# Optimization experiments

Measured on AMD Instinct MI355X. Metric: run time of the kernel, lower is better.

The kernel has to match this reference:

```python
import jax, jax.numpy as jnp
import numpy as np

D_MODEL = 1024
D_FF = 4096          # shared expert hidden
NUM_M = 2
E_ROUTER = 8 * NUM_M - 1   # 15 router experts
D_FF_R = D_FF // NUM_M     # 2048 router expert hidden
TOP_K = NUM_M * 2 - 1      # 3
B, T = 2, 2048


def setup_inputs() -> dict:
    key = jax.random.key(0)
    ks = jax.random.split(key, 12)
    s = lambda fan_in: 1.0 / np.sqrt(fan_in)
    x = jax.random.normal(ks[0], (B, T, D_MODEL), dtype=jnp.float32)
    # shared experts stacked [S=1, ...]
    sW1 = jax.random.uniform(ks[1], (1, D_MODEL, D_FF), jnp.float32, -s(D_MODEL), s(D_MODEL))
    sb1 = jax.random.uniform(ks[2], (1, D_FF), jnp.float32, -s(D_MODEL), s(D_MODEL))
    sW2 = jax.random.uniform(ks[3], (1, D_FF, D_MODEL), jnp.float32, -s(D_FF), s(D_FF))
    sb2 = jax.random.uniform(ks[4], (1, D_MODEL), jnp.float32, -s(D_FF), s(D_FF))
    # router experts stacked [E, ...]
    rW1 = jax.random.uniform(ks[5], (E_ROUTER, D_MODEL, D_FF_R), jnp.float32, -s(D_MODEL), s(D_MODEL))
    rb1 = jax.random.uniform(ks[6], (E_ROUTER, D_FF_R), jnp.float32, -s(D_MODEL), s(D_MODEL))
    rW2 = jax.random.uniform(ks[7], (E_ROUTER, D_FF_R, D_MODEL), jnp.float32, -s(D_FF_R), s(D_FF_R))
    rb2 = jax.random.uniform(ks[8], (E_ROUTER, D_MODEL), jnp.float32, -s(D_FF_R), s(D_FF_R))
    # gating linear d_model -> E
    gW = jax.random.uniform(ks[9], (D_MODEL, E_ROUTER), jnp.float32, -s(D_MODEL), s(D_MODEL))
    gb = jax.random.uniform(ks[10], (E_ROUTER,), jnp.float32, -s(D_MODEL), s(D_MODEL))
    return {"x": x, "sW1": sW1, "sb1": sb1, "sW2": sW2, "sb2": sb2,
            "rW1": rW1, "rb1": rb1, "rW2": rW2, "rb2": rb2, "gW": gW, "gb": gb}


def _expert_stack(x, W1, b1, W2, b2):
    # x: [b,t,d]; W1: [e,d,f] -> out [e,b,t,d]
    h = jax.nn.gelu(jnp.einsum('btd,edf->ebtf', x, W1) + b1[:, None, None, :],
                    approximate=False)
    return jnp.einsum('ebtf,efd->ebtd', h, W2) + b2[:, None, None, :]


def reference(x, sW1, sb1, sW2, sb2, rW1, rb1, rW2, rb2, gW, gb):
    # shared experts (sum over S)
    shared_enc = _expert_stack(x, sW1, sb1, sW2, sb2).sum(0)  # [b,t,d]
    # gating: softmax then keep top-k values (no renormalization)
    weights = jax.nn.softmax(x @ gW + gb, axis=-1)            # [b,t,E]
    topv, topi = jax.lax.top_k(weights, TOP_K)                # [b,t,K]
    gated = (jax.nn.one_hot(topi, E_ROUTER, dtype=weights.dtype)
             * topv[..., None]).sum(axis=-2)                  # [b,t,E]
    # dense per-expert compute masked by sparse gates (faithful to source)
    router_out = _expert_stack(x, rW1, rb1, rW2, rb2)         # [E,b,t,d]
    router_enc = jnp.einsum('ebtd,bte->btd', router_out, gated)
    return shared_enc + router_enc + x
```

## Files before the change

kernel.cpp:

```cpp
#include <hip/hip_runtime.h>
#include <hip/hip_bf16.h>
#include <cstdint>
#include <cstddef>

#define TOKENS 4096
#define DM     1024
#define DFF    4096
#define NE     15
#define DFR    2048
#define NEX    17
#define MAXT   104

typedef float f32x4 __attribute__((ext_vector_type(4)));
typedef int   i32x4 __attribute__((ext_vector_type(4)));

__device__ __forceinline__ void mfma_16x16x32_bf16(f32x4& d, i32x4 a, i32x4 b){
  asm("v_mfma_f32_16x16x32_bf16 %0, %1, %2, %0" : "+v"(d) : "v"(a), "v"(b));
}

__device__ __forceinline__ void gload16(const void* g, void* l){
  __builtin_amdgcn_global_load_lds(
      (const __attribute__((address_space(1))) uint32_t*)g,
      (__attribute__((address_space(3))) uint32_t*)l, 16, 0, 0);
}

__device__ __forceinline__ unsigned short f2bf(float f){
  unsigned u = __float_as_uint(f);
  u += 0x7FFFu + ((u >> 16) & 1u);
  return (unsigned short)(u >> 16);
}

__device__ __forceinline__ float gelu_exact(float v){
  return 0.5f * v * (1.0f + erff(v * 0.70710678118654752440f));
}


__global__ void cast_x_kernel(const float* __restrict__ x, ushort* __restrict__ xb, int n4){
  int i = blockIdx.x*256 + threadIdx.x;
  if (i >= n4) return;
  float4 v = reinterpret_cast<const float4*>(x)[i];
  ushort4 o; o.x=f2bf(v.x); o.y=f2bf(v.y); o.z=f2bf(v.z); o.w=f2bf(v.w);
  reinterpret_cast<ushort4*>(xb)[i] = o;
}

__global__ void tcast_kernel(const float* __restrict__ src, ushort* __restrict__ dst, int R, int C){
  __shared__ float tile[32][33];
  const size_t bo = (size_t)blockIdx.z * R * C;
  const int c0 = blockIdx.x*32, r0 = blockIdx.y*32;
  const int tx = threadIdx.x, ty = threadIdx.y;
  #pragma unroll
  for (int i=0;i<4;i++){
    int r = ty + i*8;
    tile[r][tx] = src[bo + (size_t)(r0+r)*C + c0 + tx];
  }
  __syncthreads();
  #pragma unroll
  for (int i=0;i<4;i++){
    int r = ty + i*8;
    dst[bo + (size_t)(c0+r)*R + r0 + tx] = f2bf(tile[tx][r]);
  }
}


__global__ void gate_kernel(const float* __restrict__ x, const float* __restrict__ gW,
                            const float* __restrict__ gb,
                            int* __restrict__ tokexp, float* __restrict__ tokp){
  const int wave = threadIdx.x >> 6, lane = threadIdx.x & 63;
  const int token = blockIdx.x*4 + wave;
  const float* xr = x + (size_t)token * DM;
  float a[NE];
  #pragma unroll
  for (int e=0;e<NE;e++) a[e] = 0.f;
  const int d0 = lane * 16;
  float xv[16];
  #pragma unroll
  for (int j=0;j<4;j++){
    float4 v = reinterpret_cast<const float4*>(xr + d0)[j];
    xv[j*4+0]=v.x; xv[j*4+1]=v.y; xv[j*4+2]=v.z; xv[j*4+3]=v.w;
  }
  for (int j=0;j<16;j++){
    const float* gr = gW + (size_t)(d0 + j) * NE;
    #pragma unroll
    for (int e=0;e<NE;e++) a[e] += xv[j]*gr[e];
  }
  #pragma unroll
  for (int e=0;e<NE;e++){
    for (int off=32; off; off>>=1) a[e] += __shfl_xor(a[e], off, 64);
  }
  if (lane == 0){
    float l[NE], p[NE];
    float m = -1e30f;
    for (int e=0;e<NE;e++){ l[e] = a[e] + gb[e]; m = fmaxf(m, l[e]); }
    float s = 0.f;
    for (int e=0;e<NE;e++){ p[e] = expf(l[e]-m); s += p[e]; }
    float inv = 1.f/s;
    unsigned used = 0;
    for (int k=0;k<3;k++){
      int best = -1; float bv = -1e30f;
      for (int e=0;e<NE;e++) if (!((used>>e)&1u) && l[e] > bv){ bv = l[e]; best = e; }
      used |= 1u<<best;
      tokexp[token*3 + k] = best;
      tokp[token*3 + k]   = p[best]*inv;
    }
  }
}


__global__ void assign_kernel(const int* __restrict__ tokexp, const float* __restrict__ tokp,
                              int* __restrict__ counts, int* __restrict__ bases,
                              int* __restrict__ tokidx, float* __restrict__ gatev,
                              int* __restrict__ tokslot,
                              int* __restrict__ tile_e, int* __restrict__ tile_by,
                              int* __restrict__ ntiles){
  __shared__ int lh[256][NE];
  const int tid = threadIdx.x;
  const int t0 = tid * 16;

  int le[48];
  #pragma unroll
  for (int e=0;e<NE;e++) lh[tid][e] = 0;
  #pragma unroll
  for (int j=0;j<48;j++){
    int e = tokexp[t0*3 + j];
    le[j] = e;
    lh[tid][e]++;
  }
  __syncthreads();
  if (tid < NE){
    int run = 0;
    for (int i=0;i<256;i++){
      int v = lh[i][tid];
      lh[i][tid] = run;
      run += v;
    }
    counts[tid] = run;
  }
  __syncthreads();
  if (tid == 0){
    int b = 0;
    int t = 0;
    for (int e=0;e<NE;e++){
      int c = counts[e];
      int prows = ((c+127)>>7)<<7;
      bases[e] = b; b += prows;
      int nb = (prows + 255) >> 8;
      for (int j=0;j<nb && t<MAXT;j++){ tile_e[t]=e; tile_by[t]=j; t++; }
    }
    bases[NE] = b; bases[NE+1] = b + TOKENS;
    for (int e=NE;e<NEX;e++){
      for (int j=0;j<16 && t<MAXT;j++){ tile_e[t]=e; tile_by[t]=j; t++; }
    }
    ntiles[0] = t;
  }
  __syncthreads();
  #pragma unroll
  for (int j=0;j<48;j++){
    const int t = t0 + (j/3), k = j - (j/3)*3;
    const int e = le[j];
    const int slot = lh[tid][e]++;
    const int idx = e*TOKENS + slot;
    tokidx[idx] = t;
    gatev[idx]  = tokp[t*3 + k];
    tokslot[t*3 + k] = idx;
  }
}


#define GEMM_COMPUTE(BASEB)                                                          \
  {                                                                                  \
    const char* gbase = (BASEB);                                                     \
    _Pragma("unroll")                                                                \
    for (int p=0; p<4; ++p){                                                         \
      const int qr = p>>1, qc = p&1;                                                 \
      i32x4 af[2][4], bf[2][2];                                                      \
      _Pragma("unroll")                                                              \
      for (int kk=0; kk<2; kk++){                                                    \
        const unsigned cb = (unsigned)((kk*64 + ((lane>>4)<<4)) ^ sw);               \
        _Pragma("unroll")                                                            \
        for (int m=0;m<4;m++){                                                       \
          const int row = wr*128 + qr*64 + m*16 + (lane&15);                         \
          af[kk][m] = *(const i32x4*)(gbase + row*128 + cb);                         \
        }                                                                            \
        _Pragma("unroll")                                                            \
        for (int n=0;n<2;n++){                                                       \
          const int row = wc*64 + qc*32 + n*16 + (lane&15);                          \
          bf[kk][n] = *(const i32x4*)(gbase + 32768 + row*128 + cb);                 \
        }                                                                            \
      }                                                                              \
      __builtin_amdgcn_s_setprio(1);                                                 \
      _Pragma("unroll")                                                              \
      for (int m=0;m<4;m++){                                                         \
        _Pragma("unroll")                                                            \
        for (int n=0;n<2;n++){                                                       \
          mfma_16x16x32_bf16(acc[qr*4+m][qc*2+n], af[0][m], bf[0][n]);               \
          mfma_16x16x32_bf16(acc[qr*4+m][qc*2+n], af[1][m], bf[1][n]);               \
        }                                                                            \
      }                                                                              \
      __builtin_amdgcn_s_setprio(0);                                                 \
    }                                                                                \
  }

#define GEMM_STAGE(BUF, T)                                                           \
  {                                                                                  \
    char* dA = smem + (size_t)(BUF)*65536;                                           \
    char* dB = dA + 32768;                                                           \
    _Pragma("unroll")                                                                \
    for (int i=0;i<4;i++){                                                           \
      gload16(aSrc[i] + (size_t)(T)*128, dA + i*8192 + tid*16);                      \
      gload16(bSrc[i] + (size_t)(T)*128, dB + i*8192 + tid*16);                      \
    }                                                                                \
  }


__global__ __launch_bounds__(512,2) void gemm1_kernel(
    const ushort* __restrict__ xb, const ushort* __restrict__ rW1T,
    const ushort* __restrict__ sW1T, const float* __restrict__ rb1,
    const float* __restrict__ sb1, const int* __restrict__ counts,
    const int* __restrict__ bases, const int* __restrict__ tokidx,
    const int* __restrict__ tile_e, const int* __restrict__ tile_by,
    const int* __restrict__ ntiles, ushort* __restrict__ h)
{
  const int ty = blockIdx.y;
  if (ty >= ntiles[0]) return;
  const int e = tile_e[ty], by = tile_by[ty], bx = blockIdx.x;
  const int cnt = (e < NE) ? counts[e] : TOKENS;
  const int prows = (e < NE) ? (((cnt+127)>>7)<<7) : TOKENS;

  __shared__ __align__(16) char smem[131072];

  const int tid = threadIdx.x;
  const int wave = tid >> 6, lane = tid & 63;
  const int wr = wave >> 2, wc = wave & 3;
  const unsigned sw = (unsigned)((lane & 7) << 4);

  const char* Bpb = (e < NE) ? (const char*)rW1T + ((size_t)e*DFR)*2048
                             : (const char*)sW1T + ((size_t)(e-NE)*DFR)*2048;

  const unsigned scol = (unsigned)(((tid & 7) << 4) ^ (((tid >> 3) & 7) << 4));
  const char* aSrc[4];
  const char* bSrc[4];
  #pragma unroll
  for (int i=0;i<4;i++){
    const int rl = i*64 + (tid >> 3);
    const int gr = by*256 + rl;
    int tok;
    if (e < NE){ const int cr = gr < cnt ? gr : cnt-1; tok = tokidx[e*TOKENS + cr]; }
    else       { tok = gr < TOKENS ? gr : TOKENS-1; }
    aSrc[i] = (const char*)xb + (size_t)tok*2048 + scol;
    bSrc[i] = Bpb + (size_t)(bx*256 + rl)*2048 + scol;
  }

  f32x4 acc[8][4];
  #pragma unroll
  for (int m=0;m<8;m++){
    #pragma unroll
    for (int n=0;n<4;n++){ acc[m][n] = (f32x4){0.f,0.f,0.f,0.f}; }
  }

  const int NK = DM/64;
  GEMM_STAGE(0, 0);
  asm volatile("s_waitcnt vmcnt(0)" ::: "memory");
  __builtin_amdgcn_s_barrier();
  #pragma unroll 2
  for (int t=0; t<NK-1; ++t){
    GEMM_STAGE((t+1)&1, t+1);
    asm volatile("s_waitcnt vmcnt(8)" ::: "memory");
    __builtin_amdgcn_s_barrier();
    GEMM_COMPUTE(smem + (size_t)(t&1)*65536);
    __builtin_amdgcn_s_barrier();
  }
  asm volatile("s_waitcnt vmcnt(0)" ::: "memory");
  __builtin_amdgcn_s_barrier();
  GEMM_COMPUTE(smem + (size_t)((NK-1)&1)*65536);

  const int hb = bases[e];
  const float* b1p = (e < NE) ? (rb1 + e*DFR + bx*256) : (sb1 + (e-NE)*DFR + bx*256);
  #pragma unroll
  for (int m=0;m<8;m++){
    const int rt = wr*128 + m*16 + (lane>>4)*4;
    #pragma unroll
    for (int i=0;i<4;i++){
      const int gr = by*256 + rt + i;
      if (gr < prows){
        #pragma unroll
        for (int n=0;n<4;n++){
          const int c = wc*64 + n*16 + (lane & 15);
          float v = acc[m][n][i] + b1p[c];
          h[(size_t)(hb + gr)*DFR + (size_t)bx*256 + c] = f2bf(gelu_exact(v));
        }
      }
    }
  }
}


__global__ __launch_bounds__(512,2) void gemm2_kernel(
    const ushort* __restrict__ hbuf, const ushort* __restrict__ rW2T,
    const ushort* __restrict__ sW2T, const float* __restrict__ rb2,
    const float* __restrict__ sb2, const int* __restrict__ counts,
    const int* __restrict__ bases,
    const int* __restrict__ tile_e, const int* __restrict__ tile_by,
    const int* __restrict__ ntiles, ushort* __restrict__ rout)
{
  const int ty = blockIdx.y;
  if (ty >= ntiles[0]) return;
  const int e = tile_e[ty], by = tile_by[ty], bx = blockIdx.x;
  const int cnt = (e < NE) ? counts[e] : TOKENS;
  const int prows = (e < NE) ? (((cnt+127)>>7)<<7) : TOKENS;
  const int hb = bases[e];

  __shared__ __align__(16) char smem[131072];

  const int tid = threadIdx.x;
  const int wave = tid >> 6, lane = tid & 63;
  const int wr = wave >> 2, wc = wave & 3;
  const unsigned sw = (unsigned)((lane & 7) << 4);

  const unsigned scol = (unsigned)(((tid & 7) << 4) ^ (((tid >> 3) & 7) << 4));
  const char* aSrc[4];
  const char* bSrc[4];
  #pragma unroll
  for (int i=0;i<4;i++){
    const int rl = i*64 + (tid >> 3);
    int ar = by*256 + rl; if (ar >= prows) ar = prows-1;
    aSrc[i] = (const char*)hbuf + (size_t)(hb + ar)*4096 + scol;
    if (e < NE){
      bSrc[i] = (const char*)rW2T + ((size_t)e*DM + bx*256 + rl)*4096 + scol;
    } else {
      bSrc[i] = (const char*)sW2T + (size_t)(bx*256 + rl)*8192 + (size_t)(e-NE)*4096 + scol;
    }
  }

  f32x4 acc[8][4];
  #pragma unroll
  for (int m=0;m<8;m++){
    #pragma unroll
    for (int n=0;n<4;n++){ acc[m][n] = (f32x4){0.f,0.f,0.f,0.f}; }
  }

  const int NK = DFR/64;
  GEMM_STAGE(0, 0);
  asm volatile("s_waitcnt vmcnt(0)" ::: "memory");
  __builtin_amdgcn_s_barrier();
  #pragma unroll 2
  for (int t=0; t<NK-1; ++t){
    GEMM_STAGE((t+1)&1, t+1);
    asm volatile("s_waitcnt vmcnt(8)" ::: "memory");
    __builtin_amdgcn_s_barrier();
    GEMM_COMPUTE(smem + (size_t)(t&1)*65536);
    __builtin_amdgcn_s_barrier();
  }
  asm volatile("s_waitcnt vmcnt(0)" ::: "memory");
  __builtin_amdgcn_s_barrier();
  GEMM_COMPUTE(smem + (size_t)((NK-1)&1)*65536);

  #pragma unroll
  for (int m=0;m<8;m++){
    const int rt = wr*128 + m*16 + (lane>>4)*4;
    #pragma unroll
    for (int i=0;i<4;i++){
      const int gr = by*256 + rt + i;
      if (gr < prows){
        #pragma unroll
        for (int n=0;n<4;n++){
          const int c  = wc*64 + n*16 + (lane & 15);
          const int cg = bx*256 + c;
          const float bias = (e < NE) ? rb2[e*DM + cg] : ((e == NE) ? sb2[cg] : 0.f);
          rout[(size_t)(hb + gr)*DM + cg] = f2bf(acc[m][n][i] + bias);
        }
      }
    }
  }
}


__global__ void combine_kernel(const float* __restrict__ x, const ushort* __restrict__ rout,
                               const int* __restrict__ bases, const int* __restrict__ tokslot,
                               const float* __restrict__ gatev, float* __restrict__ out)
{
  const int wave = threadIdx.x >> 6, lane = threadIdx.x & 63;
  const int token = blockIdx.x*4 + wave;
  const int d0 = lane*16;

  float acc[16];
  #pragma unroll
  for (int j=0;j<4;j++){
    float4 v = reinterpret_cast<const float4*>(x + (size_t)token*DM + d0)[j];
    acc[j*4+0]=v.x; acc[j*4+1]=v.y; acc[j*4+2]=v.z; acc[j*4+3]=v.w;
  }

  int   rows[5];
  float gs[5];
  rows[0] = bases[NE]   + token; gs[0] = 1.f;
  rows[1] = bases[NE+1] + token; gs[1] = 1.f;
  #pragma unroll
  for (int k=0;k<3;k++){
    const int idx = tokslot[token*3 + k];
    const int e = idx >> 12, s = idx & (TOKENS-1);
    rows[2+k] = bases[e] + s;
    gs[2+k] = gatev[idx];
  }

  #pragma unroll
  for (int q=0;q<5;q++){
    const float g = gs[q];
    const ushort* rp = rout + (size_t)rows[q]*DM + d0;
    #pragma unroll
    for (int h=0;h<2;h++){
      i32x4 v = *reinterpret_cast<const i32x4*>(rp + h*8);
      #pragma unroll
      for (int j=0;j<4;j++){
        const unsigned u = (unsigned)v[j];
        acc[h*8 + j*2 + 0] += g * __uint_as_float(u << 16);
        acc[h*8 + j*2 + 1] += g * __uint_as_float(u & 0xFFFF0000u);
      }
    }
  }

  #pragma unroll
  for (int j=0;j<4;j++){
    float4 v; v.x=acc[j*4+0]; v.y=acc[j*4+1]; v.z=acc[j*4+2]; v.w=acc[j*4+3];
    reinterpret_cast<float4*>(out + (size_t)token*DM + d0)[j] = v;
  }
}


extern "C" void kernel_launch(void* const* d_in, const int* in_sizes, int n_in,
                              void* d_out, int out_size, void* d_ws, size_t ws_size,
                              hipStream_t stream)
{
  (void)in_sizes; (void)n_in; (void)out_size; (void)ws_size;
  const float* x   = (const float*)d_in[0];
  const float* sW1 = (const float*)d_in[1];
  const float* sb1 = (const float*)d_in[2];
  const float* sW2 = (const float*)d_in[3];
  const float* sb2 = (const float*)d_in[4];
  const float* rW1 = (const float*)d_in[5];
  const float* rb1 = (const float*)d_in[6];
  const float* rW2 = (const float*)d_in[7];
  const float* rb2 = (const float*)d_in[8];
  const float* gW  = (const float*)d_in[9];
  const float* gb  = (const float*)d_in[10];
  float* out = (float*)d_out;

  char* ws = (char*)d_ws;
  ushort* xb   = (ushort*)(ws + 0);
  ushort* sW1T = (ushort*)(ws + 8388608);
  ushort* sW2T = (ushort*)(ws + 16777216);
  ushort* rW1T = (ushort*)(ws + 25165824);
  ushort* rW2T = (ushort*)(ws + 88080384);
  ushort* hbuf = (ushort*)(ws + 150994944);
  ushort* rout = (ushort*)(ws + 25165824);
  int*   counts  = (int*)(ws + 243269632);
  int*   bases   = (int*)(ws + 243269760);
  int*   tokidx  = (int*)(ws + 243270144);
  float* gatev   = (float*)(ws + 243515904);
  int*   tokslot = (int*)(ws + 243761664);
  int*   tokexp  = (int*)(ws + 243810816);
  float* tokp    = (float*)(ws + 243859968);
  int*   tile_e  = (int*)(ws + 243909120);
  int*   tile_by = (int*)(ws + 243910144);
  int*   ntiles  = (int*)(ws + 243911168);

  cast_x_kernel<<<dim3(TOKENS*DM/4/256), dim3(256), 0, stream>>>(x, xb, TOKENS*DM/4);
  tcast_kernel<<<dim3(DFF/32, DM/32, 1),  dim3(32,8), 0, stream>>>(sW1, sW1T, DM, DFF);
  tcast_kernel<<<dim3(DM/32, DFF/32, 1),  dim3(32,8), 0, stream>>>(sW2, sW2T, DFF, DM);
  tcast_kernel<<<dim3(DFR/32, DM/32, NE), dim3(32,8), 0, stream>>>(rW1, rW1T, DM, DFR);
  tcast_kernel<<<dim3(DM/32, DFR/32, NE), dim3(32,8), 0, stream>>>(rW2, rW2T, DFR, DM);

  gate_kernel<<<dim3(TOKENS/4), dim3(256), 0, stream>>>(x, gW, gb, tokexp, tokp);
  assign_kernel<<<dim3(1), dim3(256), 0, stream>>>(tokexp, tokp, counts, bases,
                                                   tokidx, gatev, tokslot,
                                                   tile_e, tile_by, ntiles);

  gemm1_kernel<<<dim3(8,MAXT), dim3(512), 0, stream>>>(
      xb, rW1T, sW1T, rb1, sb1, counts, bases, tokidx, tile_e, tile_by, ntiles, hbuf);
  gemm2_kernel<<<dim3(4,MAXT), dim3(512), 0, stream>>>(
      hbuf, rW2T, sW2T, rb2, sb2, counts, bases, tile_e, tile_by, ntiles, rout);
  combine_kernel<<<dim3(TOKENS/4), dim3(256), 0, stream>>>(
      x, rout, bases, tokslot, gatev, out);
}
```

Measured before the change: 491.9 us.

## Triple-buffer GEMM K-loop with smaller K tiles and 128-row gemm2 tiles

Both grouped GEMMs now use a three-stage LDS ring with K-step 32 instead of a two-stage ring with K-step 64. This keeps two loads in flight and needs only one barrier per iteration. gemm2 switches to 128-row M tiles with a separate tile list and launch bounds of 4, aiming for more blocks and higher occupancy and less padding waste. In exchange, the smaller K step adds more barriers and less MFMA work per sync, and gemm2 loses reuse of the B tile.

After: 450.9 us. -8.4%, faster.

```diff
diff --git a/kernel.cpp b/kernel.cpp
--- a/kernel.cpp
+++ b/kernel.cpp
@@ -10,6 +10,7 @@
 #define DFR    2048
 #define NEX    17
 #define MAXT   104
+#define MAXT2  176
 
 typedef float f32x4 __attribute__((ext_vector_type(4)));
 typedef int   i32x4 __attribute__((ext_vector_type(4)));
@@ -111,6 +112,7 @@
                               int* __restrict__ tokidx, float* __restrict__ gatev,
                               int* __restrict__ tokslot,
                               int* __restrict__ tile_e, int* __restrict__ tile_by,
+                              int* __restrict__ tile2_e, int* __restrict__ tile2_by,
                               int* __restrict__ ntiles){
   __shared__ int lh[256][NE];
   const int tid = threadIdx.x;
@@ -137,20 +139,22 @@
   }
   __syncthreads();
   if (tid == 0){
-    int b = 0;
-    int t = 0;
+    int b = 0, t1 = 0, t2 = 0;
     for (int e=0;e<NE;e++){
       int c = counts[e];
       int prows = ((c+127)>>7)<<7;
       bases[e] = b; b += prows;
-      int nb = (prows + 255) >> 8;
-      for (int j=0;j<nb && t<MAXT;j++){ tile_e[t]=e; tile_by[t]=j; t++; }
+      int nb1 = (prows + 255) >> 8;
+      for (int j=0;j<nb1 && t1<MAXT;j++){ tile_e[t1]=e; tile_by[t1]=j; t1++; }
+      int nb2 = prows >> 7;
+      for (int j=0;j<nb2 && t2<MAXT2;j++){ tile2_e[t2]=e; tile2_by[t2]=j; t2++; }
     }
     bases[NE] = b; bases[NE+1] = b + TOKENS;
     for (int e=NE;e<NEX;e++){
-      for (int j=0;j<16 && t<MAXT;j++){ tile_e[t]=e; tile_by[t]=j; t++; }
-    }
-    ntiles[0] = t;
+      for (int j=0;j<16 && t1<MAXT;j++){ tile_e[t1]=e; tile_by[t1]=j; t1++; }
+      for (int j=0;j<32 && t2<MAXT2;j++){ tile2_e[t2]=e; tile2_by[t2]=j; t2++; }
+    }
+    ntiles[0] = t1; ntiles[1] = t2;
   }
   __syncthreads();
   #pragma unroll
@@ -164,52 +168,6 @@
     tokslot[t*3 + k] = idx;
   }
 }
-
-
-#define GEMM_COMPUTE(BASEB)                                                          \
-  {                                                                                  \
-    const char* gbase = (BASEB);                                                     \
-    _Pragma("unroll")                                                                \
-    for (int p=0; p<4; ++p){                                                         \
-      const int qr = p>>1, qc = p&1;                                                 \
-      i32x4 af[2][4], bf[2][2];                                                      \
-      _Pragma("unroll")                                                              \
-      for (int kk=0; kk<2; kk++){                                                    \
-        const unsigned cb = (unsigned)((kk*64 + ((lane>>4)<<4)) ^ sw);               \
-        _Pragma("unroll")                                                            \
-        for (int m=0;m<4;m++){                                                       \
-          const int row = wr*128 + qr*64 + m*16 + (lane&15);                         \
-          af[kk][m] = *(const i32x4*)(gbase + row*128 + cb);                         \
-        }                                                                            \
-        _Pragma("unroll")                                                            \
-        for (int n=0;n<2;n++){                                                       \
-          const int row = wc*64 + qc*32 + n*16 + (lane&15);                          \
-          bf[kk][n] = *(const i32x4*)(gbase + 32768 + row*128 + cb);                 \
-        }                                                                            \
-      }                                                                              \
-      __builtin_amdgcn_s_setprio(1);                                                 \
-      _Pragma("unroll")                                                              \
-      for (int m=0;m<4;m++){                                                         \
-        _Pragma("unroll")                                                            \
-        for (int n=0;n<2;n++){                                                       \
-          mfma_16x16x32_bf16(acc[qr*4+m][qc*2+n], af[0][m], bf[0][n]);               \
-          mfma_16x16x32_bf16(acc[qr*4+m][qc*2+n], af[1][m], bf[1][n]);               \
-        }                                                                            \
-      }                                                                              \
-      __builtin_amdgcn_s_setprio(0);                                                 \
-    }                                                                                \
-  }
-
-#define GEMM_STAGE(BUF, T)                                                           \
-  {                                                                                  \
-    char* dA = smem + (size_t)(BUF)*65536;                                           \
-    char* dB = dA + 32768;                                                           \
-    _Pragma("unroll")                                                                \
-    for (int i=0;i<4;i++){                                                           \
-      gload16(aSrc[i] + (size_t)(T)*128, dA + i*8192 + tid*16);                      \
-      gload16(bSrc[i] + (size_t)(T)*128, dB + i*8192 + tid*16);                      \
-    }                                                                                \
-  }
 
 
 __global__ __launch_bounds__(512,2) void gemm1_kernel(
@@ -226,28 +184,26 @@
   const int cnt = (e < NE) ? counts[e] : TOKENS;
   const int prows = (e < NE) ? (((cnt+127)>>7)<<7) : TOKENS;
 
-  __shared__ __align__(16) char smem[131072];
-
-  const int tid = threadIdx.x;
-  const int wave = tid >> 6, lane = tid & 63;
+  __shared__ __align__(16) char smem[98304];
+
+  const int tid = threadIdx.x, wave = tid >> 6, lane = tid & 63;
   const int wr = wave >> 2, wc = wave & 3;
-  const unsigned sw = (unsigned)((lane & 7) << 4);
-
-  const char* Bpb = (e < NE) ? (const char*)rW1T + ((size_t)e*DFR)*2048
-                             : (const char*)sW1T + ((size_t)(e-NE)*DFR)*2048;
-
-  const unsigned scol = (unsigned)(((tid & 7) << 4) ^ (((tid >> 3) & 7) << 4));
-  const char* aSrc[4];
-  const char* bSrc[4];
-  #pragma unroll
-  for (int i=0;i<4;i++){
-    const int rl = i*64 + (tid >> 3);
+  const unsigned sc = (unsigned)(((tid & 3) ^ ((tid >> 3) & 3)) << 4);
+
+  const char* Bpb = (e < NE) ? (const char*)rW1T + (size_t)e*DFR*2048
+                             : (const char*)sW1T + (size_t)(e-NE)*DFR*2048;
+
+  const char* aSrc[2];
+  const char* bSrc[2];
+  #pragma unroll
+  for (int i=0;i<2;i++){
+    const int rl = i*128 + (tid>>2);
     const int gr = by*256 + rl;
     int tok;
     if (e < NE){ const int cr = gr < cnt ? gr : cnt-1; tok = tokidx[e*TOKENS + cr]; }
     else       { tok = gr < TOKENS ? gr : TOKENS-1; }
-    aSrc[i] = (const char*)xb + (size_t)tok*2048 + scol;
-    bSrc[i] = Bpb + (size_t)(bx*256 + rl)*2048 + scol;
+    aSrc[i] = (const char*)xb + (size_t)tok*2048 + sc;
+    bSrc[i] = Bpb + (size_t)(bx*256 + rl)*2048 + sc;
   }
 
   f32x4 acc[8][4];
@@ -257,21 +213,59 @@
     for (int n=0;n<4;n++){ acc[m][n] = (f32x4){0.f,0.f,0.f,0.f}; }
   }
 
-  const int NK = DM/64;
-  GEMM_STAGE(0, 0);
-  asm volatile("s_waitcnt vmcnt(0)" ::: "memory");
+#define G1_STAGE(BUF, T)                                                   \
+  { char* bp = smem + (BUF)*32768;                                         \
+    gload16(aSrc[0] + (T)*64, bp + tid*16);                                \
+    gload16(aSrc[1] + (T)*64, bp + 8192 + tid*16);                         \
+    gload16(bSrc[0] + (T)*64, bp + 16384 + tid*16);                        \
+    gload16(bSrc[1] + (T)*64, bp + 24576 + tid*16); }
+
+#define G1_COMPUTE(BUF)                                                    \
+  { const char* bp = smem + (BUF)*32768;                                   \
+    i32x4 bf[4];                                                           \
+    _Pragma("unroll")                                                      \
+    for (int n=0;n<4;n++){                                                 \
+      const int row = wc*64 + n*16 + (lane&15);                            \
+      bf[n] = *(const i32x4*)(bp + 16384 + row*64                          \
+               + (((lane>>4) ^ ((row>>1)&3))<<4));                         \
+    }                                                                      \
+    _Pragma("unroll")                                                      \
+    for (int q=0;q<2;q++){                                                 \
+      i32x4 af[4];                                                         \
+      _Pragma("unroll")                                                    \
+      for (int m=0;m<4;m++){                                               \
+        const int row = wr*128 + q*64 + m*16 + (lane&15);                  \
+        af[m] = *(const i32x4*)(bp + row*64                                \
+                 + (((lane>>4) ^ ((row>>1)&3))<<4));                       \
+      }                                                                    \
+      __builtin_amdgcn_s_setprio(1);                                       \
+      _Pragma("unroll")                                                    \
+      for (int m=0;m<4;m++){                                               \
+        _Pragma("unroll")                                                  \
+        for (int n=0;n<4;n++){ mfma_16x16x32_bf16(acc[q*4+m][n], af[m], bf[n]); } \
+      }                                                                    \
+      __builtin_amdgcn_s_setprio(0);                                       \
+    } }
+
+  const int NK = DM/32;
+  G1_STAGE(0, 0);
+  G1_STAGE(1, 1);
+  asm volatile("s_waitcnt vmcnt(4)" ::: "memory");
   __builtin_amdgcn_s_barrier();
-  #pragma unroll 2
-  for (int t=0; t<NK-1; ++t){
-    GEMM_STAGE((t+1)&1, t+1);
-    asm volatile("s_waitcnt vmcnt(8)" ::: "memory");
-    __builtin_amdgcn_s_barrier();
-    GEMM_COMPUTE(smem + (size_t)(t&1)*65536);
-    __builtin_amdgcn_s_barrier();
-  }
-  asm volatile("s_waitcnt vmcnt(0)" ::: "memory");
-  __builtin_amdgcn_s_barrier();
-  GEMM_COMPUTE(smem + (size_t)((NK-1)&1)*65536);
+  int cb = 0;
+  for (int t=0; t<NK; ++t){
+    if (t+2 < NK){
+      const int pb = (cb >= 1) ? cb-1 : cb+2;
+      G1_STAGE(pb, t+2);
+    }
+    G1_COMPUTE(cb);
+    if (t < NK-1){
+      if (t+2 < NK) asm volatile("s_waitcnt vmcnt(4)" ::: "memory");
+      else          asm volatile("s_waitcnt vmcnt(0)" ::: "memory");
+      __builtin_amdgcn_s_barrier();
+    }
+    cb = (cb==2) ? 0 : cb+1;
+  }
 
   const int hb = bases[e];
   const float* b1p = (e < NE) ? (rb1 + e*DFR + bx*256) : (sb1 + (e-NE)*DFR + bx*256);
@@ -291,75 +285,108 @@
       }
     }
   }
-}
-
-
-__global__ __launch_bounds__(512,2) void gemm2_kernel(
+#undef G1_STAGE
+#undef G1_COMPUTE
+}
+
+
+__global__ __launch_bounds__(512,4) void gemm2_kernel(
     const ushort* __restrict__ hbuf, const ushort* __restrict__ rW2T,
     const ushort* __restrict__ sW2T, const float* __restrict__ rb2,
     const float* __restrict__ sb2, const int* __restrict__ counts,
     const int* __restrict__ bases,
-    const int* __restrict__ tile_e, const int* __restrict__ tile_by,
+    const int* __restrict__ tile2_e, const int* __restrict__ tile2_by,
     const int* __restrict__ ntiles, ushort* __restrict__ rout)
 {
   const int ty = blockIdx.y;
-  if (ty >= ntiles[0]) return;
-  const int e = tile_e[ty], by = tile_by[ty], bx = blockIdx.x;
+  if (ty >= ntiles[1]) return;
+  const int e = tile2_e[ty], by = tile2_by[ty], bx = blockIdx.x;
   const int cnt = (e < NE) ? counts[e] : TOKENS;
   const int prows = (e < NE) ? (((cnt+127)>>7)<<7) : TOKENS;
   const int hb = bases[e];
 
-  __shared__ __align__(16) char smem[131072];
-
-  const int tid = threadIdx.x;
-  const int wave = tid >> 6, lane = tid & 63;
+  __shared__ __align__(16) char smem[73728];
+
+  const int tid = threadIdx.x, wave = tid >> 6, lane = tid & 63;
   const int wr = wave >> 2, wc = wave & 3;
-  const unsigned sw = (unsigned)((lane & 7) << 4);
-
-  const unsigned scol = (unsigned)(((tid & 7) << 4) ^ (((tid >> 3) & 7) << 4));
-  const char* aSrc[4];
-  const char* bSrc[4];
-  #pragma unroll
-  for (int i=0;i<4;i++){
-    const int rl = i*64 + (tid >> 3);
-    int ar = by*256 + rl; if (ar >= prows) ar = prows-1;
-    aSrc[i] = (const char*)hbuf + (size_t)(hb + ar)*4096 + scol;
-    if (e < NE){
-      bSrc[i] = (const char*)rW2T + ((size_t)e*DM + bx*256 + rl)*4096 + scol;
-    } else {
-      bSrc[i] = (const char*)sW2T + (size_t)(bx*256 + rl)*8192 + (size_t)(e-NE)*4096 + scol;
-    }
-  }
-
-  f32x4 acc[8][4];
-  #pragma unroll
-  for (int m=0;m<8;m++){
+  const unsigned sc = (unsigned)(((tid & 3) ^ ((tid >> 3) & 3)) << 4);
+
+  const char* aSrc;
+  {
+    const int rl = tid>>2;
+    int ar = by*128 + rl; if (ar >= prows) ar = prows-1;
+    aSrc = (const char*)hbuf + (size_t)(hb + ar)*4096 + sc;
+  }
+  const char* bSrc[2];
+  #pragma unroll
+  for (int i=0;i<2;i++){
+    const int rl = i*128 + (tid>>2);
+    if (e < NE) bSrc[i] = (const char*)rW2T + ((size_t)e*DM + bx*256 + rl)*4096 + sc;
+    else        bSrc[i] = (const char*)sW2T + (size_t)(bx*256 + rl)*8192 + (size_t)(e-NE)*4096 + sc;
+  }
+
+  f32x4 acc[4][4];
+  #pragma unroll
+  for (int m=0;m<4;m++){
     #pragma unroll
     for (int n=0;n<4;n++){ acc[m][n] = (f32x4){0.f,0.f,0.f,0.f}; }
   }
 
-  const int NK = DFR/64;
-  GEMM_STAGE(0, 0);
-  asm volatile("s_waitcnt vmcnt(0)" ::: "memory");
+#define G2_STAGE(BUF, T)                                                   \
+  { char* bp = smem + (BUF)*24576;                                         \
+    gload16(aSrc + (T)*64, bp + tid*16);                                   \
+    gload16(bSrc[0] + (T)*64, bp + 8192 + tid*16);                         \
+    gload16(bSrc[1] + (T)*64, bp + 16384 + tid*16); }
+
+#define G2_COMPUTE(BUF)                                                    \
+  { const char* bp = smem + (BUF)*24576;                                   \
+    i32x4 bf[4], af[4];                                                    \
+    _Pragma("unroll")                                                      \
+    for (int n=0;n<4;n++){                                                 \
+      const int row = wc*64 + n*16 + (lane&15);                            \
+      bf[n] = *(const i32x4*)(bp + 8192 + row*64                           \
+               + (((lane>>4) ^ ((row>>1)&3))<<4));                         \
+    }                                                                      \
+    _Pragma("unroll")                                                      \
+    for (int m=0;m<4;m++){                                                 \
+      const int row = wr*64 + m*16 + (lane&15);                            \
+      af[m] = *(const i32x4*)(bp + row*64                                  \
+               + (((lane>>4) ^ ((row>>1)&3))<<4));                         \
+    }                                                                      \
+    __builtin_amdgcn_s_setprio(1);                                         \
+    _Pragma("unroll")                                                      \
+    for (int m=0;m<4;m++){                                                 \
+      _Pragma("unroll")                                                    \
+      for (int n=0;n<4;n++){ mfma_16x16x32_bf16(acc[m][n], af[m], bf[n]); }\
+    }                                                                      \
+    __builtin_amdgcn_s_setprio(0); }
+
+  const int NK = DFR/32;
+  G2_STAGE(0, 0);
+  G2_STAGE(1, 1);
+  asm volatile("s_waitcnt vmcnt(3)" ::: "memory");
   __builtin_amdgcn_s_barrier();
-  #pragma unroll 2
-  for (int t=0; t<NK-1; ++t){
-    GEMM_STAGE((t+1)&1, t+1);
-    asm volatile("s_waitcnt vmcnt(8)" ::: "memory");
-    __builtin_amdgcn_s_barrier();
-    GEMM_COMPUTE(smem + (size_t)(t&1)*65536);
-    __builtin_amdgcn_s_barrier();
-  }
-  asm volatile("s_waitcnt vmcnt(0)" ::: "memory");
-  __builtin_amdgcn_s_barrier();
-  GEMM_COMPUTE(smem + (size_t)((NK-1)&1)*65536);
-
-  #pragma unroll
-  for (int m=0;m<8;m++){
-    const int rt = wr*128 + m*16 + (lane>>4)*4;
+  int cb = 0;
+  for (int t=0; t<NK; ++t){
+    if (t+2 < NK){
+      const int pb = (cb >= 1) ? cb-1 : cb+2;
+      G2_STAGE(pb, t+2);
+    }
+    G2_COMPUTE(cb);
+    if (t < NK-1){
+      if (t+2 < NK) asm volatile("s_waitcnt vmcnt(3)" ::: "memory");
+      else          asm volatile("s_waitcnt vmcnt(0)" ::: "memory");
+      __builtin_amdgcn_s_barrier();
+    }
+    cb = (cb==2) ? 0 : cb+1;
+  }
+
+  #pragma unroll
+  for (int m=0;m<4;m++){
+    const int rt = wr*64 + m*16 + (lane>>4)*4;
     #pragma unroll
     for (int i=0;i<4;i++){
-      const int gr = by*256 + rt + i;
+      const int gr = by*128 + rt + i;
       if (gr < prows){
         #pragma unroll
         for (int n=0;n<4;n++){
@@ -371,6 +398,8 @@
       }
     }
   }
+#undef G2_STAGE
+#undef G2_COMPUTE
 }
 
 
@@ -406,13 +435,13 @@
     const float g = gs[q];
     const ushort* rp = rout + (size_t)rows[q]*DM + d0;
     #pragma unroll
-    for (int h=0;h<2;h++){
-      i32x4 v = *reinterpret_cast<const i32x4*>(rp + h*8);
+    for (int hh=0;hh<2;hh++){
+      i32x4 v = *reinterpret_cast<const i32x4*>(rp + hh*8);
       #pragma unroll
       for (int j=0;j<4;j++){
         const unsigned u = (unsigned)v[j];
-        acc[h*8 + j*2 + 0] += g * __uint_as_float(u << 16);
-        acc[h*8 + j*2 + 1] += g * __uint_as_float(u & 0xFFFF0000u);
+        acc[hh*8 + j*2 + 0] += g * __uint_as_float(u << 16);
+        acc[hh*8 + j*2 + 1] += g * __uint_as_float(u & 0xFFFF0000u);
       }
     }
   }
@@ -461,6 +490,8 @@
   int*   tile_e  = (int*)(ws + 243909120);
   int*   tile_by = (int*)(ws + 243910144);
   int*   ntiles  = (int*)(ws + 243911168);
+  int*   tile2_e = (int*)(ws + 243912192);
+  int*   tile2_by= (int*)(ws + 243913216);
 
   cast_x_kernel<<<dim3(TOKENS*DM/4/256), dim3(256), 0, stream>>>(x, xb, TOKENS*DM/4);
   tcast_kernel<<<dim3(DFF/32, DM/32, 1),  dim3(32,8), 0, stream>>>(sW1, sW1T, DM, DFF);
@@ -471,12 +502,12 @@
   gate_kernel<<<dim3(TOKENS/4), dim3(256), 0, stream>>>(x, gW, gb, tokexp, tokp);
   assign_kernel<<<dim3(1), dim3(256), 0, stream>>>(tokexp, tokp, counts, bases,
                                                    tokidx, gatev, tokslot,
-                                                   tile_e, tile_by, ntiles);
+                                                   tile_e, tile_by, tile2_e, tile2_by, ntiles);
 
   gemm1_kernel<<<dim3(8,MAXT), dim3(512), 0, stream>>>(
       xb, rW1T, sW1T, rb1, sb1, counts, bases, tokidx, tile_e, tile_by, ntiles, hbuf);
-  gemm2_kernel<<<dim3(4,MAXT), dim3(512), 0, stream>>>(
-      hbuf, rW2T, sW2T, rb2, sb2, counts, bases, tile_e, tile_by, ntiles, rout);
+  gemm2_kernel<<<dim3(4,MAXT2), dim3(512), 0, stream>>>(
+      hbuf, rW2T, sW2T, rb2, sb2, counts, bases, tile2_e, tile2_by, ntiles, rout);
   combine_kernel<<<dim3(TOKENS/4), dim3(256), 0, stream>>>(
       x, rout, bases, tokslot, gatev, out);
 }
```
